# Kernel tuning notes

Measured on AMD Instinct MI355X. Metric: run time of the kernel, lower is better.

## Reference

```python
import jax, jax.numpy as jnp
import numpy as np

EMBED_DIM = 1024
NUM_HEADS = 8
HEAD_DIM = EMBED_DIM // NUM_HEADS


def setup_inputs() -> dict:
    key = jax.random.key(0)
    k1, k2, k3, k4, k5 = jax.random.split(key, 5)
    B, N, D = 4, 2048, EMBED_DIM
    scale = 1.0 / np.sqrt(D)
    return {
        "representation": jax.random.normal(k1, (B, N, D), dtype=jnp.float32),
        "W_qkv": jax.random.normal(k2, (D, 3 * D), dtype=jnp.float32) * scale,
        "b_qkv": jnp.zeros((3 * D,), dtype=jnp.float32),
        "W_proj": jax.random.normal(k3, (D, D), dtype=jnp.float32) * scale,
        "b_proj": jnp.zeros((D,), dtype=jnp.float32),
    }


def reference(representation, W_qkv, b_qkv, W_proj, b_proj):
    B, N, D = representation.shape
    H, Hd = NUM_HEADS, HEAD_DIM
    qkv = jnp.einsum("bnd,de->bne", representation, W_qkv) + b_qkv  # [B,N,3D]
    q, k, v = jnp.split(qkv, 3, axis=-1)
    # [B,N,D] -> [B,H,N,Hd]
    split_heads = lambda x: x.reshape(B, N, H, Hd).transpose(0, 2, 1, 3)
    q, k, v = split_heads(q), split_heads(k), split_heads(v)
    dots = jnp.einsum("bhqd,bhkd->bhqk", q, k) * (Hd ** -0.5)  # [B,H,N,N]
    attn = jax.nn.softmax(dots, axis=-1)
    out = jnp.einsum("bhqk,bhkd->bhqd", attn, v)
    out = out.transpose(0, 2, 1, 3).reshape(B, N, D)  # merge heads
    return jnp.einsum("bnd,de->bne", out, W_proj) + b_proj
```

## Files before the change

kernel.cpp:

```cpp
#include <hip/hip_runtime.h>
#include <hip/hip_bf16.h>
#include <cstdint>

typedef unsigned short u16;
typedef __attribute__((ext_vector_type(8))) short short8;
typedef __attribute__((ext_vector_type(4))) float f32x4;
typedef __attribute__((ext_vector_type(4))) unsigned short u16x4;
typedef __attribute__((ext_vector_type(4))) unsigned int u32x4;

#define NSEQ 2048
#define DMODEL 1024
#define NH 8
#define HD 128
#define KDIM 1024
#define QSCALE (0.08838834764831845f * 1.4426950408889634f)

__device__ __forceinline__ u16 f2b(float f) {
  __hip_bfloat16 h = __float2bfloat16(f);
  union { __hip_bfloat16 h; u16 u; } cv; cv.h = h; return cv.u;
}
__device__ __forceinline__ f32x4 zero4() { f32x4 z = {0.f, 0.f, 0.f, 0.f}; return z; }

__device__ __forceinline__ void gload_lds16(const u16* g, u16* l) {
  __builtin_amdgcn_global_load_lds(
      (__attribute__((address_space(1))) void*)g,
      (__attribute__((address_space(3))) void*)l, 16, 0, 0);
}

__device__ __forceinline__ int LK(int r) {
  return (r & 0x23) | ((r & 0x0C) << 1) | ((r & 0x10) >> 2);
}

__global__ void cvt_f32_bf16(const float* __restrict__ in, u16* __restrict__ out) {
  const size_t i = ((size_t)blockIdx.x * 256 + threadIdx.x) * 8;
  f32x4 a = *(const f32x4*)&in[i];
  f32x4 b = *(const f32x4*)&in[i + 4];
  short8 o;
#pragma unroll
  for (int j = 0; j < 4; ++j) { o[j] = (short)f2b(a[j]); o[4 + j] = (short)f2b(b[j]); }
  *(short8*)&out[i] = o;
}

__global__ void transpose_k(const float* __restrict__ in, u16* __restrict__ out,
                            int R, int C) {
  __shared__ u16 tile[32][33];
  const int tx = threadIdx.x, ty = threadIdx.y;
  const int c = blockIdx.x * 32 + tx;
  const int r0 = blockIdx.y * 32;
  for (int i = ty; i < 32; i += 8) tile[i][tx] = f2b(in[(size_t)(r0 + i) * C + c]);
  __syncthreads();
  const int oc = r0 + tx;
  const int c0 = blockIdx.x * 32;
  for (int i = ty; i < 32; i += 8) out[(size_t)(c0 + i) * R + oc] = tile[tx][i];
}

template <int MODE>
__global__ __launch_bounds__(256, 3) void gemm128(
    const u16* __restrict__ A, const u16* __restrict__ Bt,
    const float* __restrict__ bias, u16* __restrict__ o0,
    u16* __restrict__ o1, u16* __restrict__ o2, float* __restrict__ of) {
  __shared__ __align__(16) u16 sA[128 * 64];
  __shared__ __align__(16) u16 sB[128 * 64];

  const int tid = threadIdx.x;
  const int lane = tid & 63;
  const int w = tid >> 6;
  const int quad = lane >> 4, ln = lane & 15;
  const int m0 = blockIdx.y * 128, n0 = blockIdx.x * 128;
  const int wm = (w >> 1) * 64, wn = (w & 1) * 64;

  f32x4 acc[4][4];
#pragma unroll
  for (int i = 0; i < 4; ++i)
#pragma unroll
    for (int j = 0; j < 4; ++j) acc[i][j] = zero4();

  const int cbase = w * 4;
  for (int kb = 0; kb < KDIM / 64; ++kb) {
    __syncthreads();
    const int k0 = kb * 64;
#pragma unroll
    for (int i = 0; i < 4; ++i) {
      int c = (cbase + i) * 64 + lane;
      int r = c >> 3, s = c & 7;
      gload_lds16(A + (size_t)(m0 + r) * KDIM + k0 + s * 8, &sA[(cbase + i) * 512]);
      gload_lds16(Bt + (size_t)(n0 + r) * KDIM + k0 + s * 8, &sB[(cbase + i) * 512]);
    }
    __syncthreads();
#pragma unroll
    for (int ks = 0; ks < 2; ++ks) {
      short8 af[4], bf[4];
      const int kc = ks * 4 + quad;
#pragma unroll
      for (int t = 0; t < 4; ++t) {
        af[t] = *(const short8*)&sA[(wm + t * 16 + ln) * 64 + kc * 8];
        bf[t] = *(const short8*)&sB[(wn + t * 16 + ln) * 64 + kc * 8];
      }
#pragma unroll
      for (int mt = 0; mt < 4; ++mt)
#pragma unroll
        for (int nt = 0; nt < 4; ++nt)
          acc[mt][nt] = __builtin_amdgcn_mfma_f32_16x16x32_bf16(
              af[mt], bf[nt], acc[mt][nt], 0, 0, 0);
    }
  }

  if (MODE == 0) {
    const int which = n0 >> 10;
    const int h = (n0 & 1023) >> 7;
#pragma unroll
    for (int mt = 0; mt < 4; ++mt) {
      const int rbase = m0 + wm + mt * 16 + quad * 4;
      const int b = rbase >> 11;
      const int n = rbase & 2047;
#pragma unroll
      for (int nt = 0; nt < 4; ++nt) {
        const int dcol = wn + nt * 16 + ln;
        const float bv = bias[n0 + dcol];
        if (which == 0) {
          u16* p = o0 + ((size_t)(b * NH + h) * NSEQ + n) * HD + dcol;
#pragma unroll
          for (int rr = 0; rr < 4; ++rr)
            p[(size_t)rr * HD] = f2b((acc[mt][nt][rr] + bv) * QSCALE);
        } else if (which == 1) {
          u16* p = o1 + ((size_t)(b * NH + h) * NSEQ + n) * HD + dcol;
#pragma unroll
          for (int rr = 0; rr < 4; ++rr)
            p[(size_t)rr * HD] = f2b(acc[mt][nt][rr] + bv);
        } else {
          u16x4 pk;
#pragma unroll
          for (int rr = 0; rr < 4; ++rr) pk[rr] = f2b(acc[mt][nt][rr] + bv);
          *(u16x4*)&o2[((size_t)(b * NH + h) * HD + dcol) * NSEQ + n] = pk;
        }
      }
    }
  } else {
#pragma unroll
    for (int mt = 0; mt < 4; ++mt) {
      const int rbase = m0 + wm + mt * 16 + quad * 4;
#pragma unroll
      for (int nt = 0; nt < 4; ++nt) {
        const int col = n0 + wn + nt * 16 + ln;
        const float bv = bias[col];
#pragma unroll
        for (int rr = 0; rr < 4; ++rr)
          of[(size_t)(rbase + rr) * DMODEL + col] = acc[mt][nt][rr] + bv;
      }
    }
  }
}

__global__ __launch_bounds__(256, 2) void attn_fused(
    const u16* __restrict__ Q, const u16* __restrict__ K,
    const u16* __restrict__ Vt, u16* __restrict__ AO) {
  __shared__ __align__(16) u16 sK[2][64 * 128];
  __shared__ __align__(16) u16 sV[2][128 * 64];

  const int tid = threadIdx.x;
  const int w = tid >> 6, lane = tid & 63;
  const int quad = lane >> 4, ln = lane & 15;
  const int bh = blockIdx.y;
  const int q0 = blockIdx.x * 128;

  const u16* Qb = Q + ((size_t)bh * NSEQ + q0) * HD;
  const u16* Kb = K + (size_t)bh * NSEQ * HD;
  const u16* Vb = Vt + (size_t)bh * HD * NSEQ;

  int gk_off[4], gv_off[4];
#pragma unroll
  for (int j = 0; j < 4; ++j) {
    const int c = (w * 4 + j) * 64 + lane;
    const int rk = c >> 4, sk_ = c & 15;
    gk_off[j] = LK(rk) * HD + (sk_ ^ (rk & 7)) * 8;
    const int rv = c >> 3, sv_ = c & 7;
    gv_off[j] = rv * NSEQ + (sv_ ^ (rv & 7)) * 8;
  }

  int kbase[4], kslot[4], vfo[2][8];
#pragma unroll
  for (int n = 0; n < 4; ++n) kbase[n] = (n * 16 + ln) * 128;
#pragma unroll
  for (int ks = 0; ks < 4; ++ks)
    kslot[ks] = (((ks << 2) | quad) ^ (ln & 7)) * 8;
#pragma unroll
  for (int ks2 = 0; ks2 < 2; ++ks2)
#pragma unroll
    for (int dt = 0; dt < 8; ++dt)
      vfo[ks2][dt] = (dt * 16 + ln) * 64 + ((((ks2 << 2) | quad) ^ (ln & 7)) * 8);

  short8 qf[2][4];
#pragma unroll
  for (int mt = 0; mt < 2; ++mt)
#pragma unroll
    for (int ks = 0; ks < 4; ++ks)
      qf[mt][ks] = *(const short8*)&Qb[(size_t)(w * 32 + mt * 16 + ln) * HD +
                                       ks * 32 + quad * 8];

  f32x4 o[2][8];
#pragma unroll
  for (int mt = 0; mt < 2; ++mt)
#pragma unroll
    for (int dt = 0; dt < 8; ++dt) o[mt][dt] = zero4();
  float l_part[2] = {0.f, 0.f};

#pragma unroll
  for (int j = 0; j < 4; ++j) {
    gload_lds16(Kb + gk_off[j], &sK[0][(w * 4 + j) * 512]);
    gload_lds16(Vb + gv_off[j], &sV[0][(w * 4 + j) * 512]);
  }

  union PU { u32x4 u; short8 s; };

#pragma unroll 1
  for (int it = 0; it < NSEQ / 128; ++it) {
#pragma unroll
    for (int c2 = 0; c2 < 2; ++c2) {
      __syncthreads();

      const int kvn = it * 128 + c2 * 64 + 64;
      if (kvn < NSEQ) {
#pragma unroll
        for (int j = 0; j < 4; ++j) {
          gload_lds16(Kb + (size_t)kvn * HD + gk_off[j],
                      &sK[c2 ^ 1][(w * 4 + j) * 512]);
          gload_lds16(Vb + kvn + gv_off[j], &sV[c2 ^ 1][(w * 4 + j) * 512]);
        }
      }
      const u16* skr = &sK[c2][0];
      const u16* svr = &sV[c2][0];

      __builtin_amdgcn_s_setprio(1);

      f32x4 sacc[4][2];
      PU ph[2][2];
      short8 vf0[8], vf1[8];

      auto SM = [&](int m) {
#pragma unroll
        for (int mt = 0; mt < 2; ++mt) {
          float e0 = exp2f(sacc[m][mt][0]);
          float e1 = exp2f(sacc[m][mt][1]);
          float e2 = exp2f(sacc[m][mt][2]);
          float e3 = exp2f(sacc[m][mt][3]);
          l_part[mt] += (e0 + e1) + (e2 + e3);
          unsigned a0 = __float_as_uint(e0) + 0x8000u;
          unsigned a1 = __float_as_uint(e1) + 0x8000u;
          unsigned a2 = __float_as_uint(e2) + 0x8000u;
          unsigned a3 = __float_as_uint(e3) + 0x8000u;
          ph[mt][m >> 1].u[(m & 1) * 2 + 0] = __builtin_amdgcn_perm(a1, a0, 0x07060302);
          ph[mt][m >> 1].u[(m & 1) * 2 + 1] = __builtin_amdgcn_perm(a3, a2, 0x07060302);
        }
      };

#pragma unroll
      for (int n = 0; n < 4; ++n) {
#pragma unroll
        for (int mt = 0; mt < 2; ++mt) sacc[n][mt] = zero4();
#pragma unroll
        for (int ks = 0; ks < 4; ++ks) {
          short8 kf = *(const short8*)&skr[kbase[n] + kslot[ks]];
          sacc[n][0] = __builtin_amdgcn_mfma_f32_16x16x32_bf16(
              kf, qf[0][ks], sacc[n][0], 0, 0, 0);
          sacc[n][1] = __builtin_amdgcn_mfma_f32_16x16x32_bf16(
              kf, qf[1][ks], sacc[n][1], 0, 0, 0);
        }
        if (n == 1) {
#pragma unroll
          for (int dt = 0; dt < 4; ++dt)
            vf0[dt] = *(const short8*)&svr[vfo[0][dt]];
        } else if (n == 2) {
#pragma unroll
          for (int dt = 4; dt < 8; ++dt)
            vf0[dt] = *(const short8*)&svr[vfo[0][dt]];
        }
        if (n) SM(n - 1);
      }

      {
        short8 pf0 = ph[0][0].s, pf1 = ph[1][0].s;
#pragma unroll
        for (int dt = 0; dt < 8; ++dt) {
          o[0][dt] = __builtin_amdgcn_mfma_f32_16x16x32_bf16(
              pf0, vf0[dt], o[0][dt], 0, 0, 0);
          o[1][dt] = __builtin_amdgcn_mfma_f32_16x16x32_bf16(
              pf1, vf0[dt], o[1][dt], 0, 0, 0);
        }
      }
#pragma unroll
      for (int dt = 0; dt < 8; ++dt)
        vf1[dt] = *(const short8*)&svr[vfo[1][dt]];
      SM(3);
      {
        short8 pf0 = ph[0][1].s, pf1 = ph[1][1].s;
#pragma unroll
        for (int dt = 0; dt < 8; ++dt) {
          o[0][dt] = __builtin_amdgcn_mfma_f32_16x16x32_bf16(
              pf0, vf1[dt], o[0][dt], 0, 0, 0);
          o[1][dt] = __builtin_amdgcn_mfma_f32_16x16x32_bf16(
              pf1, vf1[dt], o[1][dt], 0, 0, 0);
        }
      }
      __builtin_amdgcn_s_setprio(0);
    }
  }

  const int b = bh >> 3, h = bh & 7;
#pragma unroll
  for (int mt = 0; mt < 2; ++mt) {
    float v = l_part[mt];
    v += __shfl_xor(v, 16, 64);
    v += __shfl_xor(v, 32, 64);
    float inv[4];
#pragma unroll
    for (int rr = 0; rr < 4; ++rr)
      inv[rr] = 1.0f / __shfl(v, quad * 4 + rr, 64);
    const int rbase = q0 + w * 32 + mt * 16 + quad * 4;
#pragma unroll
    for (int dt = 0; dt < 8; ++dt) {
      const int d = dt * 16 + ln;
#pragma unroll
      for (int rr = 0; rr < 4; ++rr)
        AO[((size_t)b * NSEQ + rbase + rr) * DMODEL + h * HD + d] =
            f2b(o[mt][dt][rr] * inv[rr]);
    }
  }
}

extern "C" void kernel_launch(void* const* d_in, const int* in_sizes, int n_in,
                              void* d_out, int out_size, void* d_ws, size_t ws_size,
                              hipStream_t stream) {
  const float* X = (const float*)d_in[0];
  const float* Wqkv = (const float*)d_in[1];
  const float* bqkv = (const float*)d_in[2];
  const float* Wproj = (const float*)d_in[3];
  const float* bproj = (const float*)d_in[4];
  float* out = (float*)d_out;

  const size_t NEED_BYTES =
      2ull * (8388608  + 3072 * 1024 + 1024 * 1024 + 3 * 8388608 + 8388608);
  if (ws_size < NEED_BYTES) return;

  u16* ws = (u16*)d_ws;
  u16* Xb = ws;
  u16* WqkvT = Xb + 8388608;
  u16* WprojT = WqkvT + 3072 * 1024;
  u16* Qb = WprojT + 1024 * 1024;
  u16* Kb = Qb + 8388608;
  u16* Vtb = Kb + 8388608;
  u16* AO = Vtb + 8388608;

  cvt_f32_bf16<<<8388608 / (256 * 8), 256, 0, stream>>>(X, Xb);
  transpose_k<<<dim3(3072 / 32, 1024 / 32), dim3(32, 8), 0, stream>>>(Wqkv, WqkvT, 1024, 3072);
  transpose_k<<<dim3(1024 / 32, 1024 / 32), dim3(32, 8), 0, stream>>>(Wproj, WprojT, 1024, 1024);
  gemm128<0><<<dim3(3072 / 128, 8192 / 128), 256, 0, stream>>>(
      Xb, WqkvT, bqkv, Qb, Kb, Vtb, nullptr);
  attn_fused<<<dim3(2048 / 128, 32), 256, 0, stream>>>(Qb, Kb, Vtb, AO);
  gemm128<1><<<dim3(1024 / 128, 8192 / 128), 256, 0, stream>>>(
      AO, WprojT, bproj, nullptr, nullptr, nullptr, out);
}
```

Measured before the change: 273.1 us.

## Rewrite projection GEMMs with double-buffered LDS pipeline, swizzle, and larger tiles

Replaces the 128x128 single-buffered GEMM with a 256x128 tile, 512-thread kernel that double-buffers LDS and issues global-to-LDS loads for the next K step while computing the current one. It also adds an XOR swizzle on LDS columns to avoid bank conflicts, an XCD-aware block-index remap for cache locality, and setprio around the MFMA bursts. The aim is to hide global load latency and cut LDS conflicts in both the QKV and output projections. In exchange it uses more LDS and relies on hand-placed waitcnt/barrier ordering, which is fragile.

```diff
diff --git a/kernel.cpp b/kernel.cpp
--- a/kernel.cpp
+++ b/kernel.cpp
@@ -55,19 +55,28 @@
 }
 
 template <int MODE>
-__global__ __launch_bounds__(256, 3) void gemm128(
+__global__ __launch_bounds__(512, 2) void gemm_pipe(
     const u16* __restrict__ A, const u16* __restrict__ Bt,
     const float* __restrict__ bias, u16* __restrict__ o0,
     u16* __restrict__ o1, u16* __restrict__ o2, float* __restrict__ of) {
-  __shared__ __align__(16) u16 sA[128 * 64];
-  __shared__ __align__(16) u16 sB[128 * 64];
+  __shared__ __align__(16) u16 sA[2][256 * 64];
+  __shared__ __align__(16) u16 sB[2][128 * 64];
 
   const int tid = threadIdx.x;
   const int lane = tid & 63;
   const int w = tid >> 6;
   const int quad = lane >> 4, ln = lane & 15;
-  const int m0 = blockIdx.y * 128, n0 = blockIdx.x * 128;
-  const int wm = (w >> 1) * 64, wn = (w & 1) * 64;
+  const int wm = w >> 1, wn = w & 1;
+
+  const int NT = (MODE == 0) ? 24 : 8;
+  const int nwg = gridDim.x, cpx = nwg >> 3;
+  const int id = blockIdx.x;
+  const int swz = (id & 7) * cpx + (id >> 3);
+  const int m0 = (swz / NT) * 256, n0 = (swz % NT) * 128;
+
+  const int r0 = tid >> 3, s0 = tid & 7;
+  const u16* aSrc = A + (size_t)(m0 + r0) * KDIM + (s0 ^ (r0 & 7)) * 8;
+  const u16* bSrc = Bt + (size_t)(n0 + r0) * KDIM + (s0 ^ (r0 & 7)) * 8;
 
   f32x4 acc[4][4];
 #pragma unroll
@@ -75,77 +84,127 @@
 #pragma unroll
     for (int j = 0; j < 4; ++j) acc[i][j] = zero4();
 
-  const int cbase = w * 4;
-  for (int kb = 0; kb < KDIM / 64; ++kb) {
-    __syncthreads();
-    const int k0 = kb * 64;
-#pragma unroll
-    for (int i = 0; i < 4; ++i) {
-      int c = (cbase + i) * 64 + lane;
-      int r = c >> 3, s = c & 7;
-      gload_lds16(A + (size_t)(m0 + r) * KDIM + k0 + s * 8, &sA[(cbase + i) * 512]);
-      gload_lds16(Bt + (size_t)(n0 + r) * KDIM + k0 + s * 8, &sB[(cbase + i) * 512]);
-    }
-    __syncthreads();
-#pragma unroll
-    for (int ks = 0; ks < 2; ++ks) {
-      short8 af[4], bf[4];
-      const int kc = ks * 4 + quad;
-#pragma unroll
-      for (int t = 0; t < 4; ++t) {
-        af[t] = *(const short8*)&sA[(wm + t * 16 + ln) * 64 + kc * 8];
-        bf[t] = *(const short8*)&sB[(wn + t * 16 + ln) * 64 + kc * 8];
-      }
-#pragma unroll
-      for (int mt = 0; mt < 4; ++mt)
-#pragma unroll
-        for (int nt = 0; nt < 4; ++nt)
-          acc[mt][nt] = __builtin_amdgcn_mfma_f32_16x16x32_bf16(
-              af[mt], bf[nt], acc[mt][nt], 0, 0, 0);
-    }
+  auto STAGE = [&](int ktn, int p) {
+    u16* dA = &sA[ktn & 1][0];
+    u16* dB = &sB[ktn & 1][0];
+    const int k0n = ktn * 64;
+    if (p == 0) {
+      gload_lds16(aSrc + k0n,                        dA + tid * 8);
+      gload_lds16(aSrc + (size_t)64 * KDIM + k0n,    dA + 64 * 64 + tid * 8);
+      gload_lds16(aSrc + (size_t)128 * KDIM + k0n,   dA + 128 * 64 + tid * 8);
+    } else {
+      gload_lds16(aSrc + (size_t)192 * KDIM + k0n,   dA + 192 * 64 + tid * 8);
+      gload_lds16(bSrc + k0n,                        dB + tid * 8);
+      gload_lds16(bSrc + (size_t)64 * KDIM + k0n,    dB + 64 * 64 + tid * 8);
+    }
+  };
+
+  STAGE(0, 0);
+  STAGE(0, 1);
+
+#pragma unroll 1
+  for (int kt = 0; kt < KDIM / 64; ++kt) {
+    const int bb = kt & 1;
+    const u16* lA = &sA[bb][0];
+    const u16* lB = &sB[bb][0];
+
+    if (kt < KDIM / 64 - 1) {
+      STAGE(kt + 1, 0);
+      asm volatile("s_waitcnt vmcnt(3)" ::: "memory");
+    } else {
+      asm volatile("s_waitcnt vmcnt(0)" ::: "memory");
+    }
+    __builtin_amdgcn_s_barrier();
+    asm volatile("" ::: "memory");
+
+    short8 af[4][2], bf[2][2];
+#pragma unroll
+    for (int mf = 0; mf < 4; ++mf)
+#pragma unroll
+      for (int kk = 0; kk < 2; ++kk)
+        af[mf][kk] = *(const short8*)&lA[(wm * 64 + mf * 16 + ln) * 64 +
+                                         ((((kk << 2) | quad)) ^ (ln & 7)) * 8];
+#pragma unroll
+    for (int nf = 0; nf < 2; ++nf)
+#pragma unroll
+      for (int kk = 0; kk < 2; ++kk)
+        bf[nf][kk] = *(const short8*)&lB[(wn * 64 + nf * 16 + ln) * 64 +
+                                         ((((kk << 2) | quad)) ^ (ln & 7)) * 8];
+    asm volatile("s_waitcnt lgkmcnt(0)" ::: "memory");
+    __builtin_amdgcn_sched_barrier(0);
+    __builtin_amdgcn_s_setprio(1);
+#pragma unroll
+    for (int kk = 0; kk < 2; ++kk)
+#pragma unroll
+      for (int mf = 0; mf < 4; ++mf)
+#pragma unroll
+        for (int nf = 0; nf < 2; ++nf)
+          acc[mf][nf] = __builtin_amdgcn_mfma_f32_16x16x32_bf16(
+              af[mf][kk], bf[nf][kk], acc[mf][nf], 0, 0, 0);
+    __builtin_amdgcn_s_setprio(0);
+
+    if (kt < KDIM / 64 - 1) STAGE(kt + 1, 1);
+#pragma unroll
+    for (int nf = 0; nf < 2; ++nf)
+#pragma unroll
+      for (int kk = 0; kk < 2; ++kk)
+        bf[nf][kk] = *(const short8*)&lB[(wn * 64 + (nf + 2) * 16 + ln) * 64 +
+                                         ((((kk << 2) | quad)) ^ (ln & 7)) * 8];
+    asm volatile("s_waitcnt lgkmcnt(0)" ::: "memory");
+    __builtin_amdgcn_sched_barrier(0);
+    __builtin_amdgcn_s_setprio(1);
+#pragma unroll
+    for (int kk = 0; kk < 2; ++kk)
+#pragma unroll
+      for (int mf = 0; mf < 4; ++mf)
+#pragma unroll
+        for (int nf = 0; nf < 2; ++nf)
+          acc[mf][nf + 2] = __builtin_amdgcn_mfma_f32_16x16x32_bf16(
+              af[mf][kk], bf[nf][kk], acc[mf][nf + 2], 0, 0, 0);
+    __builtin_amdgcn_s_setprio(0);
   }
 
   if (MODE == 0) {
     const int which = n0 >> 10;
     const int h = (n0 & 1023) >> 7;
 #pragma unroll
-    for (int mt = 0; mt < 4; ++mt) {
-      const int rbase = m0 + wm + mt * 16 + quad * 4;
+    for (int mf = 0; mf < 4; ++mf) {
+      const int rbase = m0 + wm * 64 + mf * 16 + quad * 4;
       const int b = rbase >> 11;
       const int n = rbase & 2047;
 #pragma unroll
-      for (int nt = 0; nt < 4; ++nt) {
-        const int dcol = wn + nt * 16 + ln;
+      for (int nf = 0; nf < 4; ++nf) {
+        const int dcol = wn * 64 + nf * 16 + ln;
         const float bv = bias[n0 + dcol];
         if (which == 0) {
           u16* p = o0 + ((size_t)(b * NH + h) * NSEQ + n) * HD + dcol;
 #pragma unroll
           for (int rr = 0; rr < 4; ++rr)
-            p[(size_t)rr * HD] = f2b((acc[mt][nt][rr] + bv) * QSCALE);
+            p[(size_t)rr * HD] = f2b((acc[mf][nf][rr] + bv) * QSCALE);
         } else if (which == 1) {
           u16* p = o1 + ((size_t)(b * NH + h) * NSEQ + n) * HD + dcol;
 #pragma unroll
           for (int rr = 0; rr < 4; ++rr)
-            p[(size_t)rr * HD] = f2b(acc[mt][nt][rr] + bv);
+            p[(size_t)rr * HD] = f2b(acc[mf][nf][rr] + bv);
         } else {
           u16x4 pk;
 #pragma unroll
-          for (int rr = 0; rr < 4; ++rr) pk[rr] = f2b(acc[mt][nt][rr] + bv);
+          for (int rr = 0; rr < 4; ++rr) pk[rr] = f2b(acc[mf][nf][rr] + bv);
           *(u16x4*)&o2[((size_t)(b * NH + h) * HD + dcol) * NSEQ + n] = pk;
         }
       }
     }
   } else {
 #pragma unroll
-    for (int mt = 0; mt < 4; ++mt) {
-      const int rbase = m0 + wm + mt * 16 + quad * 4;
-#pragma unroll
-      for (int nt = 0; nt < 4; ++nt) {
-        const int col = n0 + wn + nt * 16 + ln;
+    for (int mf = 0; mf < 4; ++mf) {
+      const int rbase = m0 + wm * 64 + mf * 16 + quad * 4;
+#pragma unroll
+      for (int nf = 0; nf < 4; ++nf) {
+        const int col = n0 + wn * 64 + nf * 16 + ln;
         const float bv = bias[col];
 #pragma unroll
         for (int rr = 0; rr < 4; ++rr)
-          of[(size_t)(rbase + rr) * DMODEL + col] = acc[mt][nt][rr] + bv;
+          of[(size_t)(rbase + rr) * DMODEL + col] = acc[mf][nf][rr] + bv;
       }
     }
   }
@@ -353,9 +412,7 @@
   cvt_f32_bf16<<<8388608 / (256 * 8), 256, 0, stream>>>(X, Xb);
   transpose_k<<<dim3(3072 / 32, 1024 / 32), dim3(32, 8), 0, stream>>>(Wqkv, WqkvT, 1024, 3072);
   transpose_k<<<dim3(1024 / 32, 1024 / 32), dim3(32, 8), 0, stream>>>(Wproj, WprojT, 1024, 1024);
-  gemm128<0><<<dim3(3072 / 128, 8192 / 128), 256, 0, stream>>>(
-      Xb, WqkvT, bqkv, Qb, Kb, Vtb, nullptr);
+  gemm_pipe<0><<<768, 512, 0, stream>>>(Xb, WqkvT, bqkv, Qb, Kb, Vtb, nullptr);
   attn_fused<<<dim3(2048 / 128, 32), 256, 0, stream>>>(Qb, Kb, Vtb, AO);
-  gemm128<1><<<dim3(1024 / 128, 8192 / 128), 256, 0, stream>>>(
-      AO, WprojT, bproj, nullptr, nullptr, nullptr, out);
-}
+  gemm_pipe<1><<<256, 512, 0, stream>>>(AO, WprojT, bproj, nullptr, nullptr, nullptr, out);
+}
```

New measurement: 269.8 us. About the same (-1.2%).
